# Kernel tuning notes

Measured on AMD Instinct MI355X. Metric: run time of the kernel, lower is better.

The kernel has to match this reference:

```python
import jax, jax.numpy as jnp
import numpy as np

N, E, P = 10000, 160000, 4000
ND, ED, H, C = 8, 3, 4, 64     # node_dim, edge_dim, heads, hidden_dim (=out channels/head)
D1 = H * C                     # 256, concat output of each GATv2 layer


def setup_inputs():
    key = jax.random.key(0)
    ks = jax.random.split(key, 40)
    g = lambda k, shp, s=0.05: (jax.random.normal(k, shp, jnp.float32) * s)
    x = jax.random.normal(ks[0], (N, ND), jnp.float32)
    src = jax.random.randint(ks[1], (E,), 0, N)
    dst = jax.random.randint(ks[2], (E,), 0, N)
    edge_index = jnp.stack([src, dst])                     # [2,E]
    edge_attr = jax.random.normal(ks[3], (E, ED), jnp.float32)
    physical_edges = edge_index[:, :P].T                   # [P,2], guaranteed hits
    inp = dict(x=x, edge_index=edge_index, edge_attr=edge_attr, physical_edges=physical_edges)
    # GATv2 layer 1: in ND -> H*C (lin_l, lin_r with bias; lin_edge no bias; att [H,C]; final bias)
    inp.update(Wl1=g(ks[4], (ND, H * C)), bl1=g(ks[5], (H * C,)),
               Wr1=g(ks[6], (ND, H * C)), br1=g(ks[7], (H * C,)),
               We1=g(ks[8], (ED, H * C)), att1=g(ks[9], (H, C)), b1=g(ks[10], (H * C,)))
    # GATv2 layer 2: in D1 -> H*C
    inp.update(Wl2=g(ks[11], (D1, H * C)), bl2=g(ks[12], (H * C,)),
               Wr2=g(ks[13], (D1, H * C)), br2=g(ks[14], (H * C,)),
               We2=g(ks[15], (ED, H * C)), att2=g(ks[16], (H, C)), b2=g(ks[17], (H * C,)))
    # edge_q_net: Linear(2*D1+ED -> C), Linear(C -> C//2), Linear(C//2 -> 1)
    inp.update(Wq1=g(ks[18], (2 * D1 + ED, C)), bq1=g(ks[19], (C,)),
               Wq2=g(ks[20], (C, C // 2)), bq2=g(ks[21], (C // 2,)),
               Wq3=g(ks[22], (C // 2, 1)), bq3=g(ks[23], (1,)))
    # node_q_net: Linear(D1 -> C), Linear(C -> C//2), Linear(C//2 -> 1)
    inp.update(Wn1=g(ks[24], (D1, C)), bn1=g(ks[25], (C,)),
               Wn2=g(ks[26], (C, C // 2)), bn2=g(ks[27], (C // 2,)),
               Wn3=g(ks[28], (C // 2, 1)), bn3=g(ks[29], (1,)))
    return inp


def gatv2(x, src, dst, e_attr, Wl, bl, Wr, br, We, att, bias):
    """PyG GATv2Conv with edge_dim, concat=True. Returns [N, H*C]."""
    xl = (x @ Wl + bl).reshape(-1, H, C)          # source transform  [N,H,C]
    xr = (x @ Wr + br).reshape(-1, H, C)          # target transform  [N,H,C]
    ee = (e_attr @ We).reshape(-1, H, C)          # edge transform    [E,H,C]
    m = jax.nn.leaky_relu(xl[src] + xr[dst] + ee, 0.2)   # [E,H,C]
    logits = jnp.einsum('ehc,hc->eh', m, att)            # [E,H]
    amax = jax.ops.segment_max(logits, dst, num_segments=N)
    ex = jnp.exp(logits - amax[dst])
    den = jax.ops.segment_sum(ex, dst, num_segments=N) + 1e-16
    alpha = ex / den[dst]                                 # softmax over incoming edges
    out = jax.ops.segment_sum(alpha[:, :, None] * xl[src], dst, num_segments=N)
    return out.reshape(-1, H * C) + bias


def reference(x, edge_index, edge_attr, physical_edges,
              Wl1, bl1, Wr1, br1, We1, att1, b1,
              Wl2, bl2, Wr2, br2, We2, att2, b2,
              Wq1, bq1, Wq2, bq2, Wq3, bq3,
              Wn1, bn1, Wn2, bn2, Wn3, bn3):
    src, dst = edge_index[0], edge_index[1]
    h = jax.nn.elu(gatv2(x, src, dst, edge_attr, Wl1, bl1, Wr1, br1, We1, att1, b1))
    h = jax.nn.elu(gatv2(h, src, dst, edge_attr, Wl2, bl2, Wr2, br2, We2, att2, b2))

    # vectorized replacement of the per-physical-edge Python loop:
    # first matching edge index for (i,j) or (j,i); zeros if absent.
    keys = src * N + dst                           # unique key per directed edge (fits int32)
    order = jnp.argsort(keys)                      # stable -> smallest original index first
    skeys = keys[order]
    i, j = physical_edges[:, 0], physical_edges[:, 1]

    def first_idx(q):
        pos = jnp.clip(jnp.searchsorted(skeys, q), 0, E - 1)
        fnd = skeys[pos] == q
        return jnp.where(fnd, order[pos], E), fnd   # E = sentinel (> any valid idx)

    i1, f1 = first_idx(i * N + j)
    i2, f2 = first_idx(j * N + i)
    idx = jnp.minimum(i1, i2)                       # first index of combined mask
    found = f1 | f2
    efeat = jnp.where(found[:, None], edge_attr[jnp.clip(idx, 0, E - 1)], 0.0)   # [P,ED]

    ef = jnp.concatenate([h[i], h[j], efeat], axis=-1)                # [P, 2*D1+ED]
    eq = jax.nn.elu(ef @ Wq1 + bq1)
    eq = jax.nn.elu(eq @ Wq2 + bq2)
    entangle_q = (eq @ Wq3 + bq3)[:, 0]                               # [P]

    nq = jax.nn.elu(h @ Wn1 + bn1)
    nq = jax.nn.elu(nq @ Wn2 + bn2)
    swap_q = (nq @ Wn3 + bn3)[:, 0]                                   # [N]
    return entangle_q, swap_q
```

## Files before the change

kernel.cpp:

```cpp
#include <hip/hip_runtime.h>
#include <cmath>

constexpr int kN  = 10000;
constexpr int kE  = 160000;
constexpr int kP  = 4000;
constexpr int kND = 8;
constexpr int kH  = 4;
constexpr int kC  = 64;
constexpr int kD1 = kH * kC;
constexpr int kEFS  = 2 * kD1 + 3;
constexpr int kEFSP = 544;
constexpr int kCap  = 64;

constexpr unsigned kTblSize = 1u << 19;
constexpr unsigned kTblMask = kTblSize - 1;
constexpr unsigned kEmpty   = 0xFFFFFFFFu;

typedef __attribute__((ext_vector_type(8))) short bf16x8;
typedef __attribute__((ext_vector_type(4))) float f32x4;

__device__ __forceinline__ unsigned short f2bf(float f) {
  unsigned u = __float_as_uint(f);
  unsigned r = (u + 0x7FFFu + ((u >> 16) & 1u)) >> 16;
  return (unsigned short)r;
}
__device__ __forceinline__ float bf2f(unsigned short u) {
  return __uint_as_float(((unsigned)u) << 16);
}

__device__ __forceinline__ unsigned hash_u32(unsigned k) {
  k *= 2654435761u;
  k ^= k >> 16;
  return k & kTblMask;
}

constexpr int kGemmBX    = (kN + 63) / 64;
constexpr int kGemmBlk   = kGemmBX * 8;
constexpr int kEdgeBlk   = (kE + 255) / 256;
constexpr int kCvtElems  = 2 * 256 * 256 + 64 * kEFSP + 64 * 256;
constexpr int kCvtBlk    = (kCvtElems + 255) / 256;
constexpr int kMegaBlk   = kGemmBlk + kEdgeBlk + kCvtBlk;

__launch_bounds__(256)
__global__ void mega1_k(const float* __restrict__ x,
                        const float* __restrict__ Wl1, const float* __restrict__ bl1,
                        const float* __restrict__ Wr1, const float* __restrict__ br1,
                        unsigned short* __restrict__ xl_bf, unsigned short* __restrict__ xr_bf,
                        const int* __restrict__ src, const int* __restrict__ dst,
                        const float* __restrict__ edge_attr,
                        int* __restrict__ cnt, unsigned* __restrict__ tbl,
                        float4* __restrict__ rec,
                        const float* __restrict__ Wl2, const float* __restrict__ Wr2,
                        const float* __restrict__ Wq1, const float* __restrict__ Wn1,
                        unsigned short* __restrict__ Wl2t, unsigned short* __restrict__ Wr2t,
                        unsigned short* __restrict__ Wq1t, unsigned short* __restrict__ Wn1t) {
  __shared__ __align__(16) float s_a[8][68];
  __shared__ __align__(16) float s_w[8][64];
  int bi = blockIdx.x;
  int tid = threadIdx.x;
  if (bi < kGemmBlk) {
    int bx = bi % kGemmBX, by = bi / kGemmBX;
    int r0 = bx * 64;
    const float* W; const float* bb; unsigned short* outp;
    if (by < 4) { W = Wl1; bb = bl1; outp = xl_bf; }
    else        { W = Wr1; bb = br1; outp = xr_bf; by -= 4; }
    int cbase = by * 64;
#pragma unroll
    for (int f = tid; f < 512; f += 256) {
      int rr = f >> 3, kk = f & 7;
      int r = r0 + rr;
      s_a[kk][rr] = (r < kN) ? x[(size_t)r * kND + kk] : 0.f;
    }
#pragma unroll
    for (int f = tid; f < 512; f += 256) {
      int kk = f >> 6, cc = f & 63;
      s_w[kk][cc] = W[(size_t)kk * kD1 + cbase + cc];
    }
    __syncthreads();
    int tx = tid & 15, ty = tid >> 4;
    float acc[4][4];
#pragma unroll
    for (int i = 0; i < 4; i++)
#pragma unroll
      for (int j = 0; j < 4; j++) acc[i][j] = 0.f;
#pragma unroll
    for (int kk = 0; kk < 8; kk++) {
      float4 av = *(const float4*)&s_a[kk][ty * 4];
      float4 wv = *(const float4*)&s_w[kk][tx * 4];
      float a4[4] = {av.x, av.y, av.z, av.w};
      float w4[4] = {wv.x, wv.y, wv.z, wv.w};
#pragma unroll
      for (int i = 0; i < 4; i++)
#pragma unroll
        for (int j = 0; j < 4; j++) acc[i][j] = fmaf(a4[i], w4[j], acc[i][j]);
    }
    int c = cbase + tx * 4;
    float b4[4] = {bb[c], bb[c + 1], bb[c + 2], bb[c + 3]};
#pragma unroll
    for (int i = 0; i < 4; i++) {
      int r = r0 + ty * 4 + i;
      if (r < kN) {
        ushort4 v;
        v.x = f2bf(acc[i][0] + b4[0]); v.y = f2bf(acc[i][1] + b4[1]);
        v.z = f2bf(acc[i][2] + b4[2]); v.w = f2bf(acc[i][3] + b4[3]);
        *(ushort4*)&outp[(size_t)r * kD1 + c] = v;
      }
    }
  } else if (bi < kGemmBlk + kEdgeBlk) {
    int e = (bi - kGemmBlk) * 256 + tid;
    if (e >= kE) return;
    int s = src[e], d = dst[e];
    unsigned key = (unsigned)s * (unsigned)kN + (unsigned)d;
    unsigned h = hash_u32(key);
    for (;;) {
      unsigned prev = atomicCAS(&tbl[2 * h], kEmpty, key);
      if (prev == kEmpty || prev == key) {
        atomicMin(&tbl[2 * h + 1], (unsigned)e);
        break;
      }
      h = (h + 1) & kTblMask;
    }
    int slot = atomicAdd(&cnt[d], 1) + 1;
    if (slot < kCap) {
      float4 r;
      r.x = __int_as_float(s);
      r.y = edge_attr[e * 3 + 0];
      r.z = edge_attr[e * 3 + 1];
      r.w = edge_attr[e * 3 + 2];
      rec[(size_t)d * kCap + slot] = r;
    }
  } else {
    const int s0 = 256 * 256, s1 = 2 * s0, s2 = s1 + 64 * kEFSP, s3 = s2 + 64 * 256;
    int idx = (bi - kGemmBlk - kEdgeBlk) * 256 + tid;
    if (idx < s0) {
      int n = idx >> 8, k = idx & 255;
      Wl2t[idx] = f2bf(Wl2[(size_t)k * 256 + n]);
    } else if (idx < s1) {
      int q = idx - s0;
      int n = q >> 8, k = q & 255;
      Wr2t[q] = f2bf(Wr2[(size_t)k * 256 + n]);
    } else if (idx < s2) {
      int q = idx - s1;
      int n = q / kEFSP, k = q - n * kEFSP;
      Wq1t[q] = (k < kEFS) ? f2bf(Wq1[(size_t)k * 64 + n]) : (unsigned short)0;
    } else if (idx < s3) {
      int q = idx - s2;
      int n = q >> 8, k = q & 255;
      Wn1t[q] = f2bf(Wn1[(size_t)k * 64 + n]);
    }
  }
}

template <int ACT>
__launch_bounds__(256)
__global__ void mgemm_k(const unsigned short* __restrict__ in, int M, int Kp,
                        const unsigned short* __restrict__ Wt0,
                        const float* __restrict__ b0, unsigned short* __restrict__ out0,
                        const unsigned short* __restrict__ Wt1,
                        const float* __restrict__ b1, unsigned short* __restrict__ out1,
                        int N, int nby) {
  __shared__ __align__(16) short s_a[64][32];
  __shared__ __align__(16) short s_b[64][32];
  int tid = threadIdx.x;
  int l = tid & 63, w = tid >> 6;
  int r0 = blockIdx.x * 64;
  int by = blockIdx.y;
  const unsigned short* Wt = Wt0; const float* bb = b0; unsigned short* outv = out0;
  if (by >= nby) { Wt = Wt1; bb = b1; outv = out1; by -= nby; }
  int cbase = by * 64;

  int sr = tid >> 2;
  int skc = tid & 3;

  f32x4 acc[4];
#pragma unroll
  for (int c = 0; c < 4; c++) acc[c] = (f32x4){0.f, 0.f, 0.f, 0.f};

  int m_frag = l & 15, quad = l >> 4;

  for (int k0 = 0; k0 < Kp; k0 += 32) {
    bf16x8 av = {0, 0, 0, 0, 0, 0, 0, 0};
    int r = r0 + sr;
    if (r < M) av = *(const bf16x8*)&in[(size_t)r * Kp + k0 + skc * 8];
    *(bf16x8*)&s_a[sr][skc * 8] = av;
    bf16x8 bv = *(const bf16x8*)&Wt[(size_t)(cbase + sr) * Kp + k0 + skc * 8];
    *(bf16x8*)&s_b[sr][skc * 8] = bv;
    __syncthreads();
    bf16x8 af = *(const bf16x8*)&s_a[w * 16 + m_frag][quad * 8];
#pragma unroll
    for (int c = 0; c < 4; c++) {
      bf16x8 bfr = *(const bf16x8*)&s_b[c * 16 + m_frag][quad * 8];
      acc[c] = __builtin_amdgcn_mfma_f32_16x16x32_bf16(af, bfr, acc[c], 0, 0, 0);
    }
    __syncthreads();
  }

#pragma unroll
  for (int c = 0; c < 4; c++) {
    int col = cbase + c * 16 + m_frag;
    float bv = bb[col];
#pragma unroll
    for (int i = 0; i < 4; i++) {
      int r = r0 + w * 16 + quad * 4 + i;
      if (r < M) {
        float u = acc[c][i] + bv;
        if (ACT == 1) u = (u > 0.f) ? u : expm1f(u);
        outv[(size_t)r * N + col] = f2bf(u);
      }
    }
  }
}

__launch_bounds__(256)
__global__ void gat_k(const unsigned short* __restrict__ xl_bf,
                      const unsigned short* __restrict__ xr_bf,
                      const int* __restrict__ cnt, const float4* __restrict__ rec,
                      const float* __restrict__ We, const float* __restrict__ att,
                      const float* __restrict__ bias, unsigned short* __restrict__ out_bf) {
  int tid = threadIdx.x;
  int l = tid & 63, w = tid >> 6;
  int c0 = (l >> 4) * kC + (l & 15) * 4;

  float4 we0 = *(const float4*)&We[0 * kD1 + c0];
  float4 we1 = *(const float4*)&We[1 * kD1 + c0];
  float4 we2 = *(const float4*)&We[2 * kD1 + c0];
  float4 at4 = *(const float4*)&att[c0];
  float4 b4  = *(const float4*)&bias[c0];

  int n = blockIdx.x * 4 + w;
  if (n >= kN) return;

  ushort4 xrv = *(const ushort4*)&xr_bf[(size_t)n * kD1 + c0];
  float4 xr_c = {bf2f(xrv.x), bf2f(xrv.y), bf2f(xrv.z), bf2f(xrv.w)};

  int deg = cnt[n] + 1;
  if (deg > kCap) deg = kCap;
  int row = n * kCap, end = row + deg;
  float S = 0.f;
  float A0 = 0.f, A1 = 0.f, A2 = 0.f, A3 = 0.f;

  int k = row;
  float4 rA, rB; ushort4 xA, xB;
  if (k < end) {
    rA = rec[k];
    xA = *(const ushort4*)&xl_bf[(size_t)__float_as_int(rA.x) * kD1 + c0];
  }
  if (k + 1 < end) {
    rB = rec[k + 1];
    xB = *(const ushort4*)&xl_bf[(size_t)__float_as_int(rB.x) * kD1 + c0];
  }
  for (; k < end; k++) {
    float4 rc = rA; ushort4 xc = xA;
    rA = rB; xA = xB;
    if (k + 2 < end) {
      rB = rec[k + 2];
      xB = *(const ushort4*)&xl_bf[(size_t)__float_as_int(rB.x) * kD1 + c0];
    }
    float x0 = bf2f(xc.x), x1 = bf2f(xc.y), x2 = bf2f(xc.z), x3 = bf2f(xc.w);
    float m0 = x0 + xr_c.x + fmaf(rc.y, we0.x, fmaf(rc.z, we1.x, rc.w * we2.x));
    float m1 = x1 + xr_c.y + fmaf(rc.y, we0.y, fmaf(rc.z, we1.y, rc.w * we2.y));
    float m2 = x2 + xr_c.z + fmaf(rc.y, we0.z, fmaf(rc.z, we1.z, rc.w * we2.z));
    float m3 = x3 + xr_c.w + fmaf(rc.y, we0.w, fmaf(rc.z, we1.w, rc.w * we2.w));
    m0 = fmaxf(m0, 0.2f * m0); m1 = fmaxf(m1, 0.2f * m1);
    m2 = fmaxf(m2, 0.2f * m2); m3 = fmaxf(m3, 0.2f * m3);
    float t = fmaf(m0, at4.x, fmaf(m1, at4.y, fmaf(m2, at4.z, m3 * at4.w)));
    t += __shfl_xor(t, 1);
    t += __shfl_xor(t, 2);
    t += __shfl_xor(t, 4);
    t += __shfl_xor(t, 8);
    float wgt = __expf(t);
    S += wgt;
    A0 = fmaf(wgt, x0, A0); A1 = fmaf(wgt, x1, A1);
    A2 = fmaf(wgt, x2, A2); A3 = fmaf(wgt, x3, A3);
  }
  float inv = 1.f / (S + 1e-16f);
  float u0 = fmaf(A0, inv, b4.x), u1 = fmaf(A1, inv, b4.y);
  float u2 = fmaf(A2, inv, b4.z), u3 = fmaf(A3, inv, b4.w);
  u0 = (u0 > 0.f) ? u0 : expm1f(u0);
  u1 = (u1 > 0.f) ? u1 : expm1f(u1);
  u2 = (u2 > 0.f) ? u2 : expm1f(u2);
  u3 = (u3 > 0.f) ? u3 : expm1f(u3);
  ushort4 ov;
  ov.x = f2bf(u0); ov.y = f2bf(u1); ov.z = f2bf(u2); ov.w = f2bf(u3);
  *(ushort4*)&out_bf[(size_t)n * kD1 + c0] = ov;
}

constexpr int kEheadBlk = (kP + 15) / 16;
constexpr int kNheadBlk = (kN + 15) / 16;

__launch_bounds__(256)
__global__ void heads_k(const unsigned short* __restrict__ h_bf, const int* __restrict__ pe,
                        const float* __restrict__ edge_attr, const unsigned* __restrict__ tbl,
                        const unsigned short* __restrict__ Wqt, const float* __restrict__ bq1,
                        const float* __restrict__ Wq2, const float* __restrict__ bq2,
                        const float* __restrict__ Wq3, const float* __restrict__ bq3,
                        const unsigned short* __restrict__ Wnt, const float* __restrict__ bn1,
                        const float* __restrict__ Wn2, const float* __restrict__ bn2,
                        const float* __restrict__ Wn3, const float* __restrict__ bn3,
                        float* __restrict__ out_e, float* __restrict__ out_n) {
  __shared__ union {
    struct { __align__(16) short a[16][32]; __align__(16) short b[64][32]; } st;
    float u[16][68];
  } sm;
  __shared__ int s_i[16], s_j[16];
  __shared__ unsigned short s_ea[16][4];
  int tid = threadIdx.x;
  int l = tid & 63, w = tid >> 6;
  int ar = tid >> 2, skc = tid & 3;
  int m_frag = l & 15, quad = l >> 4;

  f32x4 acc = (f32x4){0.f, 0.f, 0.f, 0.f};

  if (blockIdx.x < kEheadBlk) {
    int r0 = blockIdx.x * 16;
    if (tid < 16) {
      int p = r0 + tid;
      int i = 0, j = 0;
      unsigned short e0 = 0, e1 = 0, e2 = 0;
      if (p < kP) {
        i = pe[p * 2 + 0]; j = pe[p * 2 + 1];
        unsigned best = kEmpty;
        unsigned keys[2] = { (unsigned)i * (unsigned)kN + (unsigned)j,
                             (unsigned)j * (unsigned)kN + (unsigned)i };
        for (int q = 0; q < 2; q++) {
          unsigned key = keys[q];
          unsigned hsh = hash_u32(key);
          for (;;) {
            unsigned k2 = tbl[2 * hsh];
            if (k2 == kEmpty) break;
            if (k2 == key) {
              unsigned v = tbl[2 * hsh + 1];
              if (v < best) best = v;
              break;
            }
            hsh = (hsh + 1) & kTblMask;
          }
        }
        if (best != kEmpty) {
          e0 = f2bf(edge_attr[best * 3 + 0]);
          e1 = f2bf(edge_attr[best * 3 + 1]);
          e2 = f2bf(edge_attr[best * 3 + 2]);
        }
      }
      s_i[tid] = i; s_j[tid] = j;
      s_ea[tid][0] = e0; s_ea[tid][1] = e1; s_ea[tid][2] = e2; s_ea[tid][3] = 0;
    }
    __syncthreads();

    for (int k0 = 0; k0 < kEFSP; k0 += 32) {
      if (tid < 64) {
        int gk = k0 + skc * 8;
        bf16x8 av;
        if (gk < 256) {
          av = *(const bf16x8*)&h_bf[(size_t)s_i[ar] * kD1 + gk];
        } else if (gk < 512) {
          av = *(const bf16x8*)&h_bf[(size_t)s_j[ar] * kD1 + (gk - 256)];
        } else {
          av = (bf16x8){0, 0, 0, 0, 0, 0, 0, 0};
          if (gk == 512) {
            av[0] = (short)s_ea[ar][0];
            av[1] = (short)s_ea[ar][1];
            av[2] = (short)s_ea[ar][2];
          }
        }
        *(bf16x8*)&sm.st.a[ar][skc * 8] = av;
      }
      bf16x8 bv = *(const bf16x8*)&Wqt[(size_t)ar * kEFSP + k0 + skc * 8];
      *(bf16x8*)&sm.st.b[ar][skc * 8] = bv;
      __syncthreads();
      bf16x8 af  = *(const bf16x8*)&sm.st.a[m_frag][quad * 8];
      bf16x8 bfr = *(const bf16x8*)&sm.st.b[w * 16 + m_frag][quad * 8];
      acc = __builtin_amdgcn_mfma_f32_16x16x32_bf16(af, bfr, acc, 0, 0, 0);
      __syncthreads();
    }

    {
      int col = w * 16 + m_frag;
      float bv = bq1[col];
#pragma unroll
      for (int i = 0; i < 4; i++) {
        float u = acc[i] + bv;
        u = (u > 0.f) ? u : expm1f(u);
        sm.u[quad * 4 + i][col] = u;
      }
    }
    __syncthreads();

    int c2 = tid & 31, rb = (tid >> 5) * 2;
    float a2[2] = {0.f, 0.f};
    for (int k = 0; k < 64; k++) {
      float wv = Wq2[k * 32 + c2];
#pragma unroll
      for (int i = 0; i < 2; i++) a2[i] = fmaf(sm.u[rb + i][k], wv, a2[i]);
    }
    float w3 = Wq3[c2], bb2 = bq2[c2], bb3 = bq3[0];
#pragma unroll
    for (int i = 0; i < 2; i++) {
      float u = a2[i] + bb2;
      u = (u > 0.f) ? u : expm1f(u);
      float p = u * w3;
      p += __shfl_xor(p, 1);
      p += __shfl_xor(p, 2);
      p += __shfl_xor(p, 4);
      p += __shfl_xor(p, 8);
      p += __shfl_xor(p, 16);
      int r = r0 + rb + i;
      if (c2 == 0 && r < kP) out_e[r] = p + bb3;
    }
  } else {
    int r0 = (blockIdx.x - kEheadBlk) * 16;
    for (int k0 = 0; k0 < kD1; k0 += 32) {
      if (tid < 64) {
        bf16x8 av = {0, 0, 0, 0, 0, 0, 0, 0};
        int r = r0 + ar;
        if (r < kN) av = *(const bf16x8*)&h_bf[(size_t)r * kD1 + k0 + skc * 8];
        *(bf16x8*)&sm.st.a[ar][skc * 8] = av;
      }
      bf16x8 bv = *(const bf16x8*)&Wnt[(size_t)ar * kD1 + k0 + skc * 8];
      *(bf16x8*)&sm.st.b[ar][skc * 8] = bv;
      __syncthreads();
      bf16x8 af  = *(const bf16x8*)&sm.st.a[m_frag][quad * 8];
      bf16x8 bfr = *(const bf16x8*)&sm.st.b[w * 16 + m_frag][quad * 8];
      acc = __builtin_amdgcn_mfma_f32_16x16x32_bf16(af, bfr, acc, 0, 0, 0);
      __syncthreads();
    }

    {
      int col = w * 16 + m_frag;
      float bv = bn1[col];
#pragma unroll
      for (int i = 0; i < 4; i++) {
        float u = acc[i] + bv;
        u = (u > 0.f) ? u : expm1f(u);
        sm.u[quad * 4 + i][col] = u;
      }
    }
    __syncthreads();

    int c2 = tid & 31, rb = (tid >> 5) * 2;
    float a2[2] = {0.f, 0.f};
    for (int k = 0; k < 64; k++) {
      float wv = Wn2[k * 32 + c2];
#pragma unroll
      for (int i = 0; i < 2; i++) a2[i] = fmaf(sm.u[rb + i][k], wv, a2[i]);
    }
    float w3 = Wn3[c2], bb2 = bn2[c2], bb3 = bn3[0];
#pragma unroll
    for (int i = 0; i < 2; i++) {
      float u = a2[i] + bb2;
      u = (u > 0.f) ? u : expm1f(u);
      float p = u * w3;
      p += __shfl_xor(p, 1);
      p += __shfl_xor(p, 2);
      p += __shfl_xor(p, 4);
      p += __shfl_xor(p, 8);
      p += __shfl_xor(p, 16);
      int r = r0 + rb + i;
      if (c2 == 0 && r < kN) out_n[r] = p + bb3;
    }
  }
}

extern "C" void kernel_launch(void* const* d_in, const int* in_sizes, int n_in,
                              void* d_out, int out_size, void* d_ws, size_t ws_size,
                              hipStream_t stream) {
  const float* x          = (const float*)d_in[0];
  const int*   edge_index = (const int*)d_in[1];
  const float* edge_attr  = (const float*)d_in[2];
  const int*   pe         = (const int*)d_in[3];
  const float* Wl1 = (const float*)d_in[4];
  const float* bl1 = (const float*)d_in[5];
  const float* Wr1 = (const float*)d_in[6];
  const float* br1 = (const float*)d_in[7];
  const float* We1 = (const float*)d_in[8];
  const float* att1= (const float*)d_in[9];
  const float* b1  = (const float*)d_in[10];
  const float* Wl2 = (const float*)d_in[11];
  const float* bl2 = (const float*)d_in[12];
  const float* Wr2 = (const float*)d_in[13];
  const float* br2 = (const float*)d_in[14];
  const float* We2 = (const float*)d_in[15];
  const float* att2= (const float*)d_in[16];
  const float* b2  = (const float*)d_in[17];
  const float* Wq1 = (const float*)d_in[18];
  const float* bq1 = (const float*)d_in[19];
  const float* Wq2 = (const float*)d_in[20];
  const float* bq2 = (const float*)d_in[21];
  const float* Wq3 = (const float*)d_in[22];
  const float* bq3 = (const float*)d_in[23];
  const float* Wn1 = (const float*)d_in[24];
  const float* bn1 = (const float*)d_in[25];
  const float* Wn2 = (const float*)d_in[26];
  const float* bn2 = (const float*)d_in[27];
  const float* Wn3 = (const float*)d_in[28];
  const float* bn3 = (const float*)d_in[29];

  const int* src = edge_index;
  const int* dst = edge_index + kE;

  char* ws = (char*)d_ws;
  size_t off = 0;
  auto alloc = [&](size_t bytes) -> char* {
    char* p = ws + off;
    off += (bytes + 255) & ~(size_t)255;
    return p;
  };
  unsigned short* xl_bf = (unsigned short*)alloc((size_t)kN * kD1 * 2);
  unsigned short* xr_bf = (unsigned short*)alloc((size_t)kN * kD1 * 2);
  unsigned short* h_bf  = (unsigned short*)alloc((size_t)kN * kD1 * 2);
  unsigned short* Wl2t  = (unsigned short*)alloc((size_t)kD1 * kD1 * 2);
  unsigned short* Wr2t  = (unsigned short*)alloc((size_t)kD1 * kD1 * 2);
  unsigned short* Wq1t  = (unsigned short*)alloc((size_t)64 * kEFSP * 2);
  unsigned short* Wn1t  = (unsigned short*)alloc((size_t)64 * kD1 * 2);
  float4* rec     = (float4*)alloc((size_t)kN * kCap * 16);
  int* cnt        = (int*)alloc(kN * 4);
  unsigned* tbl   = (unsigned*)alloc((size_t)kTblSize * 2 * 4);
  size_t initBytes = ((char*)tbl - (char*)cnt) + (size_t)kTblSize * 2 * 4;

  hipMemsetAsync(cnt, 0xFF, initBytes, stream);

  mega1_k<<<kMegaBlk, 256, 0, stream>>>(x, Wl1, bl1, Wr1, br1, xl_bf, xr_bf,
                                        src, dst, edge_attr, cnt, tbl, rec,
                                        Wl2, Wr2, Wq1, Wn1,
                                        Wl2t, Wr2t, Wq1t, Wn1t);

  gat_k<<<(kN + 3) / 4, 256, 0, stream>>>(xl_bf, xr_bf, cnt, rec, We1, att1, b1, h_bf);
  mgemm_k<0><<<dim3(kGemmBX, 8), 256, 0, stream>>>(h_bf, kN, kD1,
                                                   Wl2t, bl2, xl_bf,
                                                   Wr2t, br2, xr_bf, kD1, 4);
  gat_k<<<(kN + 3) / 4, 256, 0, stream>>>(xl_bf, xr_bf, cnt, rec, We2, att2, b2, h_bf);

  heads_k<<<kEheadBlk + kNheadBlk, 256, 0, stream>>>(h_bf, pe, edge_attr, tbl,
                                                     Wq1t, bq1, Wq2, bq2, Wq3, bq3,
                                                     Wn1t, bn1, Wn2, bn2, Wn3, bn3,
                                                     (float*)d_out, (float*)d_out + kP);
}
```

Before: 238.4 us.

## Fuse Wl2/Wr2 GEMMs sharing A tile; widen heads K-step to 64

The layer-2 GEMM now computes both the lin_l and lin_r outputs in one block, so each A tile loaded into shared memory feeds two weight tiles. This halves the grid and the redundant A loads from global memory. The heads kernel moves to a 64-wide K step with two MFMAs per barrier pair, which halves the number of sync iterations. kEFSP grows to 576 to stay a multiple of 64, so Wq1t gets extra zero padding. Risks are higher register use from the doubled accumulators and fewer blocks in the GEMM.

```diff
diff --git a/kernel.cpp b/kernel.cpp
--- a/kernel.cpp
+++ b/kernel.cpp
@@ -9,7 +9,7 @@
 constexpr int kC  = 64;
 constexpr int kD1 = kH * kC;
 constexpr int kEFS  = 2 * kD1 + 3;
-constexpr int kEFSP = 544;
+constexpr int kEFSP = 576;
 constexpr int kCap  = 64;
 
 constexpr unsigned kTblSize = 1u << 19;
@@ -151,30 +151,30 @@
   }
 }
 
-template <int ACT>
 __launch_bounds__(256)
 __global__ void mgemm_k(const unsigned short* __restrict__ in, int M, int Kp,
                         const unsigned short* __restrict__ Wt0,
                         const float* __restrict__ b0, unsigned short* __restrict__ out0,
                         const unsigned short* __restrict__ Wt1,
                         const float* __restrict__ b1, unsigned short* __restrict__ out1,
-                        int N, int nby) {
+                        int N) {
   __shared__ __align__(16) short s_a[64][32];
-  __shared__ __align__(16) short s_b[64][32];
+  __shared__ __align__(16) short s_b0[64][32];
+  __shared__ __align__(16) short s_b1[64][32];
   int tid = threadIdx.x;
   int l = tid & 63, w = tid >> 6;
   int r0 = blockIdx.x * 64;
-  int by = blockIdx.y;
-  const unsigned short* Wt = Wt0; const float* bb = b0; unsigned short* outv = out0;
-  if (by >= nby) { Wt = Wt1; bb = b1; outv = out1; by -= nby; }
-  int cbase = by * 64;
+  int cbase = blockIdx.y * 64;
 
   int sr = tid >> 2;
   int skc = tid & 3;
 
-  f32x4 acc[4];
-#pragma unroll
-  for (int c = 0; c < 4; c++) acc[c] = (f32x4){0.f, 0.f, 0.f, 0.f};
+  f32x4 acc0[4], acc1[4];
+#pragma unroll
+  for (int c = 0; c < 4; c++) {
+    acc0[c] = (f32x4){0.f, 0.f, 0.f, 0.f};
+    acc1[c] = (f32x4){0.f, 0.f, 0.f, 0.f};
+  }
 
   int m_frag = l & 15, quad = l >> 4;
 
@@ -183,14 +183,18 @@
     int r = r0 + sr;
     if (r < M) av = *(const bf16x8*)&in[(size_t)r * Kp + k0 + skc * 8];
     *(bf16x8*)&s_a[sr][skc * 8] = av;
-    bf16x8 bv = *(const bf16x8*)&Wt[(size_t)(cbase + sr) * Kp + k0 + skc * 8];
-    *(bf16x8*)&s_b[sr][skc * 8] = bv;
+    *(bf16x8*)&s_b0[sr][skc * 8] =
+        *(const bf16x8*)&Wt0[(size_t)(cbase + sr) * Kp + k0 + skc * 8];
+    *(bf16x8*)&s_b1[sr][skc * 8] =
+        *(const bf16x8*)&Wt1[(size_t)(cbase + sr) * Kp + k0 + skc * 8];
     __syncthreads();
     bf16x8 af = *(const bf16x8*)&s_a[w * 16 + m_frag][quad * 8];
 #pragma unroll
     for (int c = 0; c < 4; c++) {
-      bf16x8 bfr = *(const bf16x8*)&s_b[c * 16 + m_frag][quad * 8];
-      acc[c] = __builtin_amdgcn_mfma_f32_16x16x32_bf16(af, bfr, acc[c], 0, 0, 0);
+      bf16x8 bf0 = *(const bf16x8*)&s_b0[c * 16 + m_frag][quad * 8];
+      acc0[c] = __builtin_amdgcn_mfma_f32_16x16x32_bf16(af, bf0, acc0[c], 0, 0, 0);
+      bf16x8 bf1 = *(const bf16x8*)&s_b1[c * 16 + m_frag][quad * 8];
+      acc1[c] = __builtin_amdgcn_mfma_f32_16x16x32_bf16(af, bf1, acc1[c], 0, 0, 0);
     }
     __syncthreads();
   }
@@ -198,14 +202,13 @@
 #pragma unroll
   for (int c = 0; c < 4; c++) {
     int col = cbase + c * 16 + m_frag;
-    float bv = bb[col];
+    float bv0 = b0[col], bv1 = b1[col];
 #pragma unroll
     for (int i = 0; i < 4; i++) {
       int r = r0 + w * 16 + quad * 4 + i;
       if (r < M) {
-        float u = acc[c][i] + bv;
-        if (ACT == 1) u = (u > 0.f) ? u : expm1f(u);
-        outv[(size_t)r * N + col] = f2bf(u);
+        out0[(size_t)r * N + col] = f2bf(acc0[c][i] + bv0);
+        out1[(size_t)r * N + col] = f2bf(acc1[c][i] + bv1);
       }
     }
   }
@@ -299,15 +302,16 @@
                         const float* __restrict__ Wn3, const float* __restrict__ bn3,
                         float* __restrict__ out_e, float* __restrict__ out_n) {
   __shared__ union {
-    struct { __align__(16) short a[16][32]; __align__(16) short b[64][32]; } st;
+    struct { __align__(16) short a[16][64]; __align__(16) short b[64][64]; } st;
     float u[16][68];
   } sm;
   __shared__ int s_i[16], s_j[16];
   __shared__ unsigned short s_ea[16][4];
   int tid = threadIdx.x;
   int l = tid & 63, w = tid >> 6;
-  int ar = tid >> 2, skc = tid & 3;
   int m_frag = l & 15, quad = l >> 4;
+  int ar = tid >> 3, kg = tid & 7;
+  int br = tid >> 3;
 
   f32x4 acc = (f32x4){0.f, 0.f, 0.f, 0.f};
 
@@ -347,9 +351,9 @@
     }
     __syncthreads();
 
-    for (int k0 = 0; k0 < kEFSP; k0 += 32) {
-      if (tid < 64) {
-        int gk = k0 + skc * 8;
+    for (int k0 = 0; k0 < kEFSP; k0 += 64) {
+      if (tid < 128) {
+        int gk = k0 + kg * 8;
         bf16x8 av;
         if (gk < 256) {
           av = *(const bf16x8*)&h_bf[(size_t)s_i[ar] * kD1 + gk];
@@ -363,14 +367,22 @@
             av[2] = (short)s_ea[ar][2];
           }
         }
-        *(bf16x8*)&sm.st.a[ar][skc * 8] = av;
-      }
-      bf16x8 bv = *(const bf16x8*)&Wqt[(size_t)ar * kEFSP + k0 + skc * 8];
-      *(bf16x8*)&sm.st.b[ar][skc * 8] = bv;
+        *(bf16x8*)&sm.st.a[ar][kg * 8] = av;
+      }
+#pragma unroll
+      for (int j = 0; j < 2; j++) {
+        int idx = tid + j * 256;
+        int r2 = idx >> 3, g2 = idx & 7;
+        *(bf16x8*)&sm.st.b[r2][g2 * 8] =
+            *(const bf16x8*)&Wqt[(size_t)r2 * kEFSP + k0 + g2 * 8];
+      }
       __syncthreads();
-      bf16x8 af  = *(const bf16x8*)&sm.st.a[m_frag][quad * 8];
-      bf16x8 bfr = *(const bf16x8*)&sm.st.b[w * 16 + m_frag][quad * 8];
-      acc = __builtin_amdgcn_mfma_f32_16x16x32_bf16(af, bfr, acc, 0, 0, 0);
+#pragma unroll
+      for (int half = 0; half < 2; half++) {
+        bf16x8 af  = *(const bf16x8*)&sm.st.a[m_frag][half * 32 + quad * 8];
+        bf16x8 bfr = *(const bf16x8*)&sm.st.b[w * 16 + m_frag][half * 32 + quad * 8];
+        acc = __builtin_amdgcn_mfma_f32_16x16x32_bf16(af, bfr, acc, 0, 0, 0);
+      }
       __syncthreads();
     }
 
@@ -409,19 +421,27 @@
     }
   } else {
     int r0 = (blockIdx.x - kEheadBlk) * 16;
-    for (int k0 = 0; k0 < kD1; k0 += 32) {
-      if (tid < 64) {
+    for (int k0 = 0; k0 < kD1; k0 += 64) {
+      if (tid < 128) {
         bf16x8 av = {0, 0, 0, 0, 0, 0, 0, 0};
         int r = r0 + ar;
-        if (r < kN) av = *(const bf16x8*)&h_bf[(size_t)r * kD1 + k0 + skc * 8];
-        *(bf16x8*)&sm.st.a[ar][skc * 8] = av;
-      }
-      bf16x8 bv = *(const bf16x8*)&Wnt[(size_t)ar * kD1 + k0 + skc * 8];
-      *(bf16x8*)&sm.st.b[ar][skc * 8] = bv;
+        if (r < kN) av = *(const bf16x8*)&h_bf[(size_t)r * kD1 + k0 + kg * 8];
+        *(bf16x8*)&sm.st.a[ar][kg * 8] = av;
+      }
+#pragma unroll
+      for (int j = 0; j < 2; j++) {
+        int idx = tid + j * 256;
+        int r2 = idx >> 3, g2 = idx & 7;
+        *(bf16x8*)&sm.st.b[r2][g2 * 8] =
+            *(const bf16x8*)&Wnt[(size_t)r2 * kD1 + k0 + g2 * 8];
+      }
       __syncthreads();
-      bf16x8 af  = *(const bf16x8*)&sm.st.a[m_frag][quad * 8];
-      bf16x8 bfr = *(const bf16x8*)&sm.st.b[w * 16 + m_frag][quad * 8];
-      acc = __builtin_amdgcn_mfma_f32_16x16x32_bf16(af, bfr, acc, 0, 0, 0);
+#pragma unroll
+      for (int half = 0; half < 2; half++) {
+        bf16x8 af  = *(const bf16x8*)&sm.st.a[m_frag][half * 32 + quad * 8];
+        bf16x8 bfr = *(const bf16x8*)&sm.st.b[w * 16 + m_frag][half * 32 + quad * 8];
+        acc = __builtin_amdgcn_mfma_f32_16x16x32_bf16(af, bfr, acc, 0, 0, 0);
+      }
       __syncthreads();
     }
 
@@ -525,9 +545,9 @@
                                         Wl2t, Wr2t, Wq1t, Wn1t);
 
   gat_k<<<(kN + 3) / 4, 256, 0, stream>>>(xl_bf, xr_bf, cnt, rec, We1, att1, b1, h_bf);
-  mgemm_k<0><<<dim3(kGemmBX, 8), 256, 0, stream>>>(h_bf, kN, kD1,
-                                                   Wl2t, bl2, xl_bf,
-                                                   Wr2t, br2, xr_bf, kD1, 4);
+  mgemm_k<<<dim3(kGemmBX, 4), 256, 0, stream>>>(h_bf, kN, kD1,
+                                                Wl2t, bl2, xl_bf,
+                                                Wr2t, br2, xr_bf, kD1);
   gat_k<<<(kN + 3) / 4, 256, 0, stream>>>(xl_bf, xr_bf, cnt, rec, We2, att2, b2, h_bf);
 
   heads_k<<<kEheadBlk + kNheadBlk, 256, 0, stream>>>(h_bf, pe, edge_attr, tbl,
```

After: 230.8 us. -3.2%, faster.

## Load GEMM fragments directly into registers and compute both weight sets per block

Applied to the files above, without the earlier changes.

The layer-2 GEMM drops its LDS staging and per-k-step barriers. Each wave now holds its full 256-wide A row fragment in registers and reads B fragments straight from global memory. One block computes both the Wl2 and Wr2 outputs, so the grid's y dimension drops from 8 to 4 and every A load is reused twice. The heads kernel's edge and node MLP first layers get the same register-resident, barrier-free treatment. This raises register pressure and moves B reads to uncoalesced per-lane global loads that depend on cache.

```diff
diff --git a/kernel.cpp b/kernel.cpp
--- a/kernel.cpp
+++ b/kernel.cpp
@@ -151,61 +151,55 @@
   }
 }
 
-template <int ACT>
 __launch_bounds__(256)
-__global__ void mgemm_k(const unsigned short* __restrict__ in, int M, int Kp,
+__global__ void mgemm_k(const unsigned short* __restrict__ in, int M,
                         const unsigned short* __restrict__ Wt0,
                         const float* __restrict__ b0, unsigned short* __restrict__ out0,
                         const unsigned short* __restrict__ Wt1,
-                        const float* __restrict__ b1, unsigned short* __restrict__ out1,
-                        int N, int nby) {
-  __shared__ __align__(16) short s_a[64][32];
-  __shared__ __align__(16) short s_b[64][32];
+                        const float* __restrict__ b1, unsigned short* __restrict__ out1) {
   int tid = threadIdx.x;
   int l = tid & 63, w = tid >> 6;
+  int m_frag = l & 15, quad = l >> 4;
   int r0 = blockIdx.x * 64;
-  int by = blockIdx.y;
-  const unsigned short* Wt = Wt0; const float* bb = b0; unsigned short* outv = out0;
-  if (by >= nby) { Wt = Wt1; bb = b1; outv = out1; by -= nby; }
-  int cbase = by * 64;
-
-  int sr = tid >> 2;
-  int skc = tid & 3;
-
-  f32x4 acc[4];
-#pragma unroll
-  for (int c = 0; c < 4; c++) acc[c] = (f32x4){0.f, 0.f, 0.f, 0.f};
-
-  int m_frag = l & 15, quad = l >> 4;
-
-  for (int k0 = 0; k0 < Kp; k0 += 32) {
-    bf16x8 av = {0, 0, 0, 0, 0, 0, 0, 0};
-    int r = r0 + sr;
-    if (r < M) av = *(const bf16x8*)&in[(size_t)r * Kp + k0 + skc * 8];
-    *(bf16x8*)&s_a[sr][skc * 8] = av;
-    bf16x8 bv = *(const bf16x8*)&Wt[(size_t)(cbase + sr) * Kp + k0 + skc * 8];
-    *(bf16x8*)&s_b[sr][skc * 8] = bv;
-    __syncthreads();
-    bf16x8 af = *(const bf16x8*)&s_a[w * 16 + m_frag][quad * 8];
+  int cbase = blockIdx.y * 64;
+
+  int arow = r0 + w * 16 + m_frag;
+  bool aok = arow < M;
+  const unsigned short* ap = &in[(size_t)arow * kD1 + quad * 8];
+
+  bf16x8 a_[8];
+#pragma unroll
+  for (int s = 0; s < 8; s++)
+    a_[s] = aok ? *(const bf16x8*)&ap[s * 32] : (bf16x8){0, 0, 0, 0, 0, 0, 0, 0};
+
+  f32x4 acc0[4], acc1[4];
+#pragma unroll
+  for (int c = 0; c < 4; c++) {
+    acc0[c] = (f32x4){0.f, 0.f, 0.f, 0.f};
+    acc1[c] = (f32x4){0.f, 0.f, 0.f, 0.f};
+  }
+
+#pragma unroll
+  for (int s = 0; s < 8; s++) {
 #pragma unroll
     for (int c = 0; c < 4; c++) {
-      bf16x8 bfr = *(const bf16x8*)&s_b[c * 16 + m_frag][quad * 8];
-      acc[c] = __builtin_amdgcn_mfma_f32_16x16x32_bf16(af, bfr, acc[c], 0, 0, 0);
-    }
-    __syncthreads();
+      bf16x8 bf0 = *(const bf16x8*)&Wt0[(size_t)(cbase + c * 16 + m_frag) * kD1 + s * 32 + quad * 8];
+      acc0[c] = __builtin_amdgcn_mfma_f32_16x16x32_bf16(a_[s], bf0, acc0[c], 0, 0, 0);
+      bf16x8 bf1 = *(const bf16x8*)&Wt1[(size_t)(cbase + c * 16 + m_frag) * kD1 + s * 32 + quad * 8];
+      acc1[c] = __builtin_amdgcn_mfma_f32_16x16x32_bf16(a_[s], bf1, acc1[c], 0, 0, 0);
+    }
   }
 
 #pragma unroll
   for (int c = 0; c < 4; c++) {
     int col = cbase + c * 16 + m_frag;
-    float bv = bb[col];
+    float bv0 = b0[col], bv1 = b1[col];
 #pragma unroll
     for (int i = 0; i < 4; i++) {
       int r = r0 + w * 16 + quad * 4 + i;
       if (r < M) {
-        float u = acc[c][i] + bv;
-        if (ACT == 1) u = (u > 0.f) ? u : expm1f(u);
-        outv[(size_t)r * N + col] = f2bf(u);
+        out0[(size_t)r * kD1 + col] = f2bf(acc0[c][i] + bv0);
+        out1[(size_t)r * kD1 + col] = f2bf(acc1[c][i] + bv1);
       }
     }
   }
@@ -298,15 +292,11 @@
                         const float* __restrict__ Wn2, const float* __restrict__ bn2,
                         const float* __restrict__ Wn3, const float* __restrict__ bn3,
                         float* __restrict__ out_e, float* __restrict__ out_n) {
-  __shared__ union {
-    struct { __align__(16) short a[16][32]; __align__(16) short b[64][32]; } st;
-    float u[16][68];
-  } sm;
+  __shared__ float s_u[16][68];
   __shared__ int s_i[16], s_j[16];
   __shared__ unsigned short s_ea[16][4];
   int tid = threadIdx.x;
   int l = tid & 63, w = tid >> 6;
-  int ar = tid >> 2, skc = tid & 3;
   int m_frag = l & 15, quad = l >> 4;
 
   f32x4 acc = (f32x4){0.f, 0.f, 0.f, 0.f};
@@ -347,32 +337,36 @@
     }
     __syncthreads();
 
-    for (int k0 = 0; k0 < kEFSP; k0 += 32) {
-      if (tid < 64) {
-        int gk = k0 + skc * 8;
-        bf16x8 av;
-        if (gk < 256) {
-          av = *(const bf16x8*)&h_bf[(size_t)s_i[ar] * kD1 + gk];
-        } else if (gk < 512) {
-          av = *(const bf16x8*)&h_bf[(size_t)s_j[ar] * kD1 + (gk - 256)];
-        } else {
-          av = (bf16x8){0, 0, 0, 0, 0, 0, 0, 0};
-          if (gk == 512) {
-            av[0] = (short)s_ea[ar][0];
-            av[1] = (short)s_ea[ar][1];
-            av[2] = (short)s_ea[ar][2];
-          }
-        }
-        *(bf16x8*)&sm.st.a[ar][skc * 8] = av;
-      }
-      bf16x8 bv = *(const bf16x8*)&Wqt[(size_t)ar * kEFSP + k0 + skc * 8];
-      *(bf16x8*)&sm.st.b[ar][skc * 8] = bv;
-      __syncthreads();
-      bf16x8 af  = *(const bf16x8*)&sm.st.a[m_frag][quad * 8];
-      bf16x8 bfr = *(const bf16x8*)&sm.st.b[w * 16 + m_frag][quad * 8];
-      acc = __builtin_amdgcn_mfma_f32_16x16x32_bf16(af, bfr, acc, 0, 0, 0);
-      __syncthreads();
-    }
+    int ri = s_i[m_frag], rj = s_j[m_frag];
+    const unsigned short* bp = &Wqt[(size_t)(w * 16 + m_frag) * kEFSP + quad * 8];
+    const unsigned short* ai = &h_bf[(size_t)ri * kD1 + quad * 8];
+    const unsigned short* aj = &h_bf[(size_t)rj * kD1 + quad * 8];
+
+    bf16x8 aA[8], bA[8], aB[8], bB[8];
+#pragma unroll
+    for (int s = 0; s < 8; s++) {
+      aA[s] = *(const bf16x8*)&ai[s * 32];
+      bA[s] = *(const bf16x8*)&bp[s * 32];
+    }
+#pragma unroll
+    for (int s = 0; s < 8; s++) {
+      aB[s] = *(const bf16x8*)&aj[s * 32];
+      bB[s] = *(const bf16x8*)&bp[256 + s * 32];
+    }
+#pragma unroll
+    for (int s = 0; s < 8; s++)
+      acc = __builtin_amdgcn_mfma_f32_16x16x32_bf16(aA[s], bA[s], acc, 0, 0, 0);
+    bf16x8 a2 = (bf16x8){0, 0, 0, 0, 0, 0, 0, 0};
+    if (quad == 0) {
+      a2[0] = (short)s_ea[m_frag][0];
+      a2[1] = (short)s_ea[m_frag][1];
+      a2[2] = (short)s_ea[m_frag][2];
+    }
+    bf16x8 b2 = *(const bf16x8*)&bp[512];
+#pragma unroll
+    for (int s = 0; s < 8; s++)
+      acc = __builtin_amdgcn_mfma_f32_16x16x32_bf16(aB[s], bB[s], acc, 0, 0, 0);
+    acc = __builtin_amdgcn_mfma_f32_16x16x32_bf16(a2, b2, acc, 0, 0, 0);
 
     {
       int col = w * 16 + m_frag;
@@ -381,22 +375,22 @@
       for (int i = 0; i < 4; i++) {
         float u = acc[i] + bv;
         u = (u > 0.f) ? u : expm1f(u);
-        sm.u[quad * 4 + i][col] = u;
+        s_u[quad * 4 + i][col] = u;
       }
     }
     __syncthreads();
 
     int c2 = tid & 31, rb = (tid >> 5) * 2;
-    float a2[2] = {0.f, 0.f};
+    float a2r[2] = {0.f, 0.f};
     for (int k = 0; k < 64; k++) {
       float wv = Wq2[k * 32 + c2];
 #pragma unroll
-      for (int i = 0; i < 2; i++) a2[i] = fmaf(sm.u[rb + i][k], wv, a2[i]);
+      for (int i = 0; i < 2; i++) a2r[i] = fmaf(s_u[rb + i][k], wv, a2r[i]);
     }
     float w3 = Wq3[c2], bb2 = bq2[c2], bb3 = bq3[0];
 #pragma unroll
     for (int i = 0; i < 2; i++) {
-      float u = a2[i] + bb2;
+      float u = a2r[i] + bb2;
       u = (u > 0.f) ? u : expm1f(u);
       float p = u * w3;
       p += __shfl_xor(p, 1);
@@ -409,21 +403,17 @@
     }
   } else {
     int r0 = (blockIdx.x - kEheadBlk) * 16;
-    for (int k0 = 0; k0 < kD1; k0 += 32) {
-      if (tid < 64) {
-        bf16x8 av = {0, 0, 0, 0, 0, 0, 0, 0};
-        int r = r0 + ar;
-        if (r < kN) av = *(const bf16x8*)&h_bf[(size_t)r * kD1 + k0 + skc * 8];
-        *(bf16x8*)&sm.st.a[ar][skc * 8] = av;
-      }
-      bf16x8 bv = *(const bf16x8*)&Wnt[(size_t)ar * kD1 + k0 + skc * 8];
-      *(bf16x8*)&sm.st.b[ar][skc * 8] = bv;
-      __syncthreads();
-      bf16x8 af  = *(const bf16x8*)&sm.st.a[m_frag][quad * 8];
-      bf16x8 bfr = *(const bf16x8*)&sm.st.b[w * 16 + m_frag][quad * 8];
-      acc = __builtin_amdgcn_mfma_f32_16x16x32_bf16(af, bfr, acc, 0, 0, 0);
-      __syncthreads();
-    }
+    const unsigned short* ap = &h_bf[(size_t)(r0 + m_frag) * kD1 + quad * 8];
+    const unsigned short* bp = &Wnt[(size_t)(w * 16 + m_frag) * kD1 + quad * 8];
+    bf16x8 a_[8], b_[8];
+#pragma unroll
+    for (int s = 0; s < 8; s++) {
+      a_[s] = *(const bf16x8*)&ap[s * 32];
+      b_[s] = *(const bf16x8*)&bp[s * 32];
+    }
+#pragma unroll
+    for (int s = 0; s < 8; s++)
+      acc = __builtin_amdgcn_mfma_f32_16x16x32_bf16(a_[s], b_[s], acc, 0, 0, 0);
 
     {
       int col = w * 16 + m_frag;
@@ -432,22 +422,22 @@
       for (int i = 0; i < 4; i++) {
         float u = acc[i] + bv;
         u = (u > 0.f) ? u : expm1f(u);
-        sm.u[quad * 4 + i][col] = u;
+        s_u[quad * 4 + i][col] = u;
       }
     }
     __syncthreads();
 
     int c2 = tid & 31, rb = (tid >> 5) * 2;
-    float a2[2] = {0.f, 0.f};
+    float a2r[2] = {0.f, 0.f};
     for (int k = 0; k < 64; k++) {
       float wv = Wn2[k * 32 + c2];
 #pragma unroll
-      for (int i = 0; i < 2; i++) a2[i] = fmaf(sm.u[rb + i][k], wv, a2[i]);
+      for (int i = 0; i < 2; i++) a2r[i] = fmaf(s_u[rb + i][k], wv, a2r[i]);
     }
     float w3 = Wn3[c2], bb2 = bn2[c2], bb3 = bn3[0];
 #pragma unroll
     for (int i = 0; i < 2; i++) {
-      float u = a2[i] + bb2;
+      float u = a2r[i] + bb2;
       u = (u > 0.f) ? u : expm1f(u);
       float p = u * w3;
       p += __shfl_xor(p, 1);
@@ -525,9 +515,9 @@
                                         Wl2t, Wr2t, Wq1t, Wn1t);
 
   gat_k<<<(kN + 3) / 4, 256, 0, stream>>>(xl_bf, xr_bf, cnt, rec, We1, att1, b1, h_bf);
-  mgemm_k<0><<<dim3(kGemmBX, 8), 256, 0, stream>>>(h_bf, kN, kD1,
-                                                   Wl2t, bl2, xl_bf,
-                                                   Wr2t, br2, xr_bf, kD1, 4);
+  mgemm_k<<<dim3(kGemmBX, 4), 256, 0, stream>>>(h_bf, kN,
+                                                Wl2t, bl2, xl_bf,
+                                                Wr2t, br2, xr_bf);
   gat_k<<<(kN + 3) / 4, 256, 0, stream>>>(xl_bf, xr_bf, cnt, rec, We2, att2, b2, h_bf);
 
   heads_k<<<kEheadBlk + kNheadBlk, 256, 0, stream>>>(h_bf, pe, edge_attr, tbl,
```

After: 251.1 us. +5.3%, slower.
